# Kernel optimization log

Measured on AMD Instinct MI355X. Metric: run time of the kernel, lower is better.

Reference implementation:

```python
import jax, jax.numpy as jnp
import numpy as np

NUM_HEADS = 16


def sinusoidal_pe(N, C, dtype=jnp.float32):
    # matches the numpy construction in get_positional_encoding
    pos = jnp.arange(N, dtype=dtype)[:, None]                  # [N,1]
    dims = jnp.arange(C)                                        # [C]
    rates = 1.0 / jnp.power(jnp.asarray(10000.0, dtype), (2 * (dims // 2)).astype(dtype) / C)
    ang = pos * rates                                           # [N,C]
    pe = jnp.where(dims % 2 == 0, jnp.sin(ang), jnp.cos(ang))
    return pe.astype(dtype)


def setup_inputs() -> dict:
    key = jax.random.key(0)
    k1, k2, k3 = jax.random.split(key, 3)
    B, N, C = 4, 2048, 1024
    inputs = jax.random.normal(k1, (B, N, C), dtype=jnp.float32)
    mask_mat = jax.random.uniform(k2, (B, N), dtype=jnp.float32)
    # Glorot-uniform qkv kernel [C, 3C]
    limit = float(np.sqrt(6.0 / (C + 3 * C)))
    W_qkv = jax.random.uniform(k3, (C, 3 * C), dtype=jnp.float32, minval=-limit, maxval=limit)
    return {"inputs": inputs, "mask_mat": mask_mat, "W_qkv": W_qkv}


def reference(inputs, mask_mat, W_qkv):
    B, N, C = inputs.shape
    H = NUM_HEADS
    hd = C // H
    scale = hd ** (-0.5)

    # additive mask: -(m outer m), broadcast over heads
    neg_mask = -(mask_mat[:, :, None] * mask_mat[:, None, :])   # [B,N,N]

    x = inputs + sinusoidal_pe(N, C, inputs.dtype)              # APE
    qkv = jnp.einsum('bnc,cd->bnd', x, W_qkv)                   # [B,N,3C]
    qkv = qkv.reshape(B, N, 3, H, hd).transpose(2, 0, 3, 1, 4)  # [3,B,H,N,hd]
    q, k, v = qkv[0], qkv[1], qkv[2]

    attn = jnp.einsum('bhnd,bhmd->bhnm', q, k) * scale          # [B,H,N,N]
    attn = attn + neg_mask[:, None, :, :]
    attn = jax.nn.softmax(attn, axis=-1)
    out = jnp.einsum('bhnm,bhmd->bhnd', attn, v)                # [B,H,N,hd]
    return out.transpose(0, 2, 1, 3).reshape(B, N, C)
```

## Files before the change

kernel.cpp:

```cpp
#include <hip/hip_runtime.h>
#include <hip/hip_bf16.h>

typedef unsigned short u16;
typedef __bf16 bf16x8 __attribute__((ext_vector_type(8)));
typedef float floatx4 __attribute__((ext_vector_type(4)));

#define B_ 4
#define N_ 2048
#define C_ 1024
#define H_ 16
#define HD_ 64

__device__ __forceinline__ float b2f(u16 u) {
    union { float f; unsigned int i; } v; v.i = ((unsigned int)u) << 16; return v.f;
}
__device__ __forceinline__ u16 f2b(float f) {
    union { float f; unsigned int i; } v; v.f = f;
    unsigned int i = v.i;
    unsigned int r = i + 0x7FFFu + ((i >> 16) & 1u);
    return (u16)(r >> 16);
}
__device__ __forceinline__ unsigned int pk2(float a, float b) {
    __hip_bfloat162 t = __float22bfloat162_rn(float2{a, b});
    unsigned int u; __builtin_memcpy(&u, &t, 4); return u;
}
__device__ __forceinline__ void async16(const u16* g, u16* l) {
    __builtin_amdgcn_global_load_lds((const __attribute__((address_space(1))) unsigned int*)g,
                                     (__attribute__((address_space(3))) unsigned int*)l,
                                     16, 0, 0);
}

__global__ __launch_bounds__(256) void pe_add_kernel(const float* __restrict__ in,
                                                     u16* __restrict__ x) {
    int idx = blockIdx.x * 256 + threadIdx.x;
    int cp  = idx & 511;
    int row = idx >> 9;
    int n   = row & (N_ - 1);
    float r = exp2f(-13.287712379549449f * ((float)cp * (1.0f / 512.0f)));
    float ang = (float)n * r;
    float s, c;
    sincosf(ang, &s, &c);
    float2 pr = ((const float2*)in)[idx];
    unsigned int o = ((unsigned int)f2b(pr.y + c) << 16) | (unsigned int)f2b(pr.x + s);
    ((unsigned int*)x)[idx] = o;
}

__global__ __launch_bounds__(256) void wt_kernel(const float* __restrict__ W,
                                                 u16* __restrict__ Wt) {
    __shared__ u16 tile[32][33];
    int bx = blockIdx.x;
    int by = blockIdx.y;
    int tx = threadIdx.x & 31;
    int ty = threadIdx.x >> 5;
    for (int i = 0; i < 32; i += 8)
        tile[ty + i][tx] = f2b(W[(size_t)(by * 32 + ty + i) * 3072 + bx * 32 + tx]);
    __syncthreads();
    for (int i = 0; i < 32; i += 8)
        Wt[(size_t)(bx * 32 + ty + i) * 1024 + by * 32 + tx] = tile[tx][ty + i];
}

__global__ __launch_bounds__(256) void qkv_gemm_kernel(const u16* __restrict__ X,
                                                       const u16* __restrict__ Wt,
                                                       u16* __restrict__ q,
                                                       u16* __restrict__ k,
                                                       u16* __restrict__ vt) {
    __shared__ u16 As[128 * 64];
    __shared__ u16 Bs[128 * 64];
    int tid  = threadIdx.x;
    int wave = tid >> 6, lane = tid & 63, l15 = lane & 15, quad = lane >> 4;
    int m0 = blockIdx.x * 128;
    int n0 = blockIdx.y * 128;
    int wm = (wave & 1) * 64;
    int wn = (wave >> 1) * 64;

    floatx4 acc[4][4];
    for (int i = 0; i < 4; i++)
        for (int j = 0; j < 4; j++)
            acc[i][j] = floatx4{0.f, 0.f, 0.f, 0.f};

    int rowOff = wave * 32 + (lane >> 3);
    int colSw  = ((lane & 7) ^ (lane >> 3)) * 8;
    const u16* gA = X  + (size_t)(m0 + rowOff) * 1024 + colSw;
    const u16* gB = Wt + (size_t)(n0 + rowOff) * 1024 + colSw;
    u16* lA = As + wave * 2048;
    u16* lB = Bs + wave * 2048;

    int swl = l15 & 7;
    int aB0 = (wm + l15) * 64 + ((quad ^ swl) * 8);
    int aB1 = (wm + l15) * 64 + (((4 + quad) ^ swl) * 8);
    int bB0 = (wn + l15) * 64 + ((quad ^ swl) * 8);
    int bB1 = (wn + l15) * 64 + (((4 + quad) ^ swl) * 8);

    for (int k0 = 0; k0 < 1024; k0 += 64) {
        __syncthreads();
        async16(gA + k0,             lA);
        async16(gA + k0 +  8 * 1024, lA + 512);
        async16(gA + k0 + 16 * 1024, lA + 1024);
        async16(gA + k0 + 24 * 1024, lA + 1536);
        async16(gB + k0,             lB);
        async16(gB + k0 +  8 * 1024, lB + 512);
        async16(gB + k0 + 16 * 1024, lB + 1024);
        async16(gB + k0 + 24 * 1024, lB + 1536);
        __syncthreads();

        bf16x8 af[4][2], bf[4][2];
        for (int i = 0; i < 4; i++) {
            af[i][0] = *(const bf16x8*)(As + aB0 + i * 16 * 64);
            af[i][1] = *(const bf16x8*)(As + aB1 + i * 16 * 64);
        }
        for (int j = 0; j < 4; j++) {
            bf[j][0] = *(const bf16x8*)(Bs + bB0 + j * 16 * 64);
            bf[j][1] = *(const bf16x8*)(Bs + bB1 + j * 16 * 64);
        }
        for (int i = 0; i < 4; i++)
            for (int j = 0; j < 4; j++) {
                acc[i][j] = __builtin_amdgcn_mfma_f32_16x16x32_bf16(af[i][0], bf[j][0], acc[i][j], 0, 0, 0);
                acc[i][j] = __builtin_amdgcn_mfma_f32_16x16x32_bf16(af[i][1], bf[j][1], acc[i][j], 0, 0, 0);
            }
    }

    const float QSC = 0.125f * 1.44269504f;
    for (int i = 0; i < 4; i++) {
        int gm   = m0 + wm + i * 16 + quad * 4;
        int b    = gm >> 11;
        int nloc = gm & 2047;
        for (int j = 0; j < 4; j++) {
            int gn    = n0 + wn + j * 16 + l15;
            int which = gn >> 10;
            int cc    = gn & 1023;
            int h     = cc >> 6;
            int d     = cc & 63;
            size_t bh = (size_t)(b * 16 + h);
            if (which == 2) {
                ushort4 w4;
                w4.x = f2b(acc[i][j][0]);
                w4.y = f2b(acc[i][j][1]);
                w4.z = f2b(acc[i][j][2]);
                w4.w = f2b(acc[i][j][3]);
                *(ushort4*)(vt + (bh * 64 + d) * 2048 + nloc) = w4;
            } else {
                u16* dst = (which == 0) ? q : k;
                float sc = (which == 0) ? QSC : 1.0f;
                for (int r = 0; r < 4; r++)
                    dst[(bh * 2048 + nloc + r) * 64 + d] = f2b(acc[i][j][r] * sc);
            }
        }
    }
}

__global__ __launch_bounds__(256, 4) void attn_kernel(const u16* __restrict__ q,
                                                      const u16* __restrict__ k,
                                                      const u16* __restrict__ vt,
                                                      const float* __restrict__ mask,
                                                      float* __restrict__ out) {
    __shared__ u16 Ks[64 * 72];
    __shared__ u16 Vs[64 * 72];
    __shared__ u16 Ps[4][32 * 72];

    int tid  = threadIdx.x;
    int wave = tid >> 6, lane = tid & 63, l15 = lane & 15, quad = lane >> 4;
    int bh = blockIdx.y, b = bh >> 4, h = bh & 15;
    size_t base = (size_t)bh * (N_ * 64);
    int q0 = blockIdx.x * 128 + wave * 32;
    const float* mkb = mask + b * N_;

    bf16x8 qf[2][2];
    for (int s = 0; s < 2; s++)
        for (int dc = 0; dc < 2; dc++)
            qf[s][dc] = *(const bf16x8*)(q + base + (size_t)(q0 + s * 16 + l15) * 64 + dc * 32 + quad * 8);

    const float L2E = 1.44269504f;
    float nmq[2];
    nmq[0] = -L2E * mkb[q0 + l15];
    nmq[1] = -L2E * mkb[q0 + 16 + l15];

    floatx4 acc[2][4];
    for (int s = 0; s < 2; s++)
        for (int dt = 0; dt < 4; dt++)
            acc[s][dt] = floatx4{0.f, 0.f, 0.f, 0.f};
    float lp[2] = {0.f, 0.f};

    int r_st = tid >> 2;
    int c_st = (tid & 3) * 16;
    u16* Pw = Ps[wave];

    for (int kt = 0; kt < N_; kt += 64) {
        int4 ka = *(const int4*)(k  + base + (size_t)(kt + r_st) * 64 + c_st);
        int4 kb = *(const int4*)(k  + base + (size_t)(kt + r_st) * 64 + c_st + 8);
        int4 va = *(const int4*)(vt + ((size_t)bh * 64 + r_st) * 2048 + kt + c_st);
        int4 vb = *(const int4*)(vt + ((size_t)bh * 64 + r_st) * 2048 + kt + c_st + 8);
        float4 mkv[4];
        for (int t = 0; t < 4; t++)
            mkv[t] = *(const float4*)(mkb + kt + t * 16 + quad * 4);
        __syncthreads();
        *(int4*)(Ks + r_st * 72 + c_st)     = ka;
        *(int4*)(Ks + r_st * 72 + c_st + 8) = kb;
        *(int4*)(Vs + r_st * 72 + c_st)     = va;
        *(int4*)(Vs + r_st * 72 + c_st + 8) = vb;
        __syncthreads();

        for (int t = 0; t < 4; t++) {
            bf16x8 kf0 = *(const bf16x8*)(Ks + (t * 16 + l15) * 72 + quad * 8);
            bf16x8 kf1 = *(const bf16x8*)(Ks + (t * 16 + l15) * 72 + 32 + quad * 8);
            for (int s = 0; s < 2; s++) {
                floatx4 sa = floatx4{0.f, 0.f, 0.f, 0.f};
                sa = __builtin_amdgcn_mfma_f32_16x16x32_bf16(kf0, qf[s][0], sa, 0, 0, 0);
                sa = __builtin_amdgcn_mfma_f32_16x16x32_bf16(kf1, qf[s][1], sa, 0, 0, 0);
                float p0 = exp2f(fmaf(nmq[s], mkv[t].x, sa[0]));
                float p1 = exp2f(fmaf(nmq[s], mkv[t].y, sa[1]));
                float p2 = exp2f(fmaf(nmq[s], mkv[t].z, sa[2]));
                float p3 = exp2f(fmaf(nmq[s], mkv[t].w, sa[3]));
                lp[s] += (p0 + p1) + (p2 + p3);
                uint2 w; w.x = pk2(p0, p1); w.y = pk2(p2, p3);
                *(uint2*)(Pw + (s * 16 + l15) * 72 + t * 16 + quad * 4) = w;
            }
        }

        bf16x8 pf[2][2];
        for (int s = 0; s < 2; s++) {
            pf[s][0] = *(const bf16x8*)(Pw + (s * 16 + l15) * 72 + quad * 8);
            pf[s][1] = *(const bf16x8*)(Pw + (s * 16 + l15) * 72 + 32 + quad * 8);
        }
        for (int dt = 0; dt < 4; dt++) {
            bf16x8 vf0 = *(const bf16x8*)(Vs + (dt * 16 + l15) * 72 + quad * 8);
            bf16x8 vf1 = *(const bf16x8*)(Vs + (dt * 16 + l15) * 72 + 32 + quad * 8);
            for (int s = 0; s < 2; s++) {
                acc[s][dt] = __builtin_amdgcn_mfma_f32_16x16x32_bf16(pf[s][0], vf0, acc[s][dt], 0, 0, 0);
                acc[s][dt] = __builtin_amdgcn_mfma_f32_16x16x32_bf16(pf[s][1], vf1, acc[s][dt], 0, 0, 0);
            }
        }
    }

    for (int s = 0; s < 2; s++) {
        float lf = lp[s];
        lf += __shfl_xor(lf, 16);
        lf += __shfl_xor(lf, 32);
        float invl = 1.0f / lf;
        for (int r = 0; r < 4; r++) {
            float ir = __shfl(invl, (lane & 48) | (quad * 4 + r));
            int qrow = q0 + s * 16 + quad * 4 + r;
            float* orow = out + ((size_t)(b * N_ + qrow)) * C_ + h * 64;
            for (int dt = 0; dt < 4; dt++)
                orow[dt * 16 + l15] = acc[s][dt][r] * ir;
        }
    }
}

extern "C" void kernel_launch(void* const* d_in, const int* in_sizes, int n_in,
                              void* d_out, int out_size, void* d_ws, size_t ws_size,
                              hipStream_t stream) {
    const float* inp  = (const float*)d_in[0];
    const float* mask = (const float*)d_in[1];
    const float* W    = (const float*)d_in[2];
    float* out = (float*)d_out;

    char* ws = (char*)d_ws;
    u16* x  = (u16*)ws;
    u16* Wt = (u16*)(ws + 16777216);
    u16* q  = (u16*)(ws + 23068672);
    u16* k  = q + 8388608;
    u16* vt = k + 8388608;

    pe_add_kernel<<<16384, 256, 0, stream>>>(inp, x);
    wt_kernel<<<dim3(96, 32), 256, 0, stream>>>(W, Wt);
    qkv_gemm_kernel<<<dim3(64, 24), 256, 0, stream>>>(x, Wt, q, k, vt);
    attn_kernel<<<dim3(16, 64), 256, 0, stream>>>(q, k, vt, mask, out);
}
```

Before: 270.2 us.

## Double-buffer K/V tiles in attention and double per-wave query rows

The attention kernel now double-buffers K and V tiles in shared memory. The next tile is prefetched into registers while the current one is used, which cuts the loop to one barrier per iteration. Each wave now handles 64 query rows instead of 32, so each K/V tile is reused across twice as many rows, and the grid is halved to 512 blocks. In exchange it uses more registers and LDS, drops the occupancy hint to 2 blocks per SM, and leaves fewer blocks to fill the GPU.

```diff
diff --git a/kernel.cpp b/kernel.cpp
--- a/kernel.cpp
+++ b/kernel.cpp
@@ -148,90 +148,109 @@
     }
 }
 
-__global__ __launch_bounds__(256, 4) void attn_kernel(const u16* __restrict__ q,
+__global__ __launch_bounds__(256, 2) void attn_kernel(const u16* __restrict__ q,
                                                       const u16* __restrict__ k,
                                                       const u16* __restrict__ vt,
                                                       const float* __restrict__ mask,
                                                       float* __restrict__ out) {
-    __shared__ u16 Ks[64 * 72];
-    __shared__ u16 Vs[64 * 72];
-    __shared__ u16 Ps[4][32 * 72];
+    __shared__ u16 Ks[2][64 * 72];
+    __shared__ u16 Vs[2][64 * 72];
+    __shared__ u16 Ps[4][64 * 72];
 
     int tid  = threadIdx.x;
     int wave = tid >> 6, lane = tid & 63, l15 = lane & 15, quad = lane >> 4;
     int bh = blockIdx.y, b = bh >> 4, h = bh & 15;
     size_t base = (size_t)bh * (N_ * 64);
-    int q0 = blockIdx.x * 128 + wave * 32;
+    int q0 = blockIdx.x * 256 + wave * 64;
     const float* mkb = mask + b * N_;
 
-    bf16x8 qf[2][2];
-    for (int s = 0; s < 2; s++)
+    bf16x8 qf[4][2];
+    for (int s = 0; s < 4; s++)
         for (int dc = 0; dc < 2; dc++)
             qf[s][dc] = *(const bf16x8*)(q + base + (size_t)(q0 + s * 16 + l15) * 64 + dc * 32 + quad * 8);
 
     const float L2E = 1.44269504f;
-    float nmq[2];
-    nmq[0] = -L2E * mkb[q0 + l15];
-    nmq[1] = -L2E * mkb[q0 + 16 + l15];
-
-    floatx4 acc[2][4];
-    for (int s = 0; s < 2; s++)
+    float nmq[4];
+    for (int s = 0; s < 4; s++)
+        nmq[s] = -L2E * mkb[q0 + s * 16 + l15];
+
+    floatx4 acc[4][4];
+    for (int s = 0; s < 4; s++)
         for (int dt = 0; dt < 4; dt++)
             acc[s][dt] = floatx4{0.f, 0.f, 0.f, 0.f};
-    float lp[2] = {0.f, 0.f};
+    float lp[4] = {0.f, 0.f, 0.f, 0.f};
 
     int r_st = tid >> 2;
     int c_st = (tid & 3) * 16;
     u16* Pw = Ps[wave];
+    const u16* kgb = k  + base + (size_t)r_st * 64 + c_st;
+    const u16* vgb = vt + ((size_t)bh * 64 + r_st) * 2048 + c_st;
+
+    int4 ka, kb, va, vb;
+    ka = *(const int4*)(kgb);          kb = *(const int4*)(kgb + 8);
+    va = *(const int4*)(vgb);          vb = *(const int4*)(vgb + 8);
+    *(int4*)(Ks[0] + r_st * 72 + c_st)     = ka;
+    *(int4*)(Ks[0] + r_st * 72 + c_st + 8) = kb;
+    *(int4*)(Vs[0] + r_st * 72 + c_st)     = va;
+    *(int4*)(Vs[0] + r_st * 72 + c_st + 8) = vb;
+    ka = *(const int4*)(kgb + (size_t)64 * 64);  kb = *(const int4*)(kgb + (size_t)64 * 64 + 8);
+    va = *(const int4*)(vgb + 64);               vb = *(const int4*)(vgb + 64 + 8);
+    __syncthreads();
 
     for (int kt = 0; kt < N_; kt += 64) {
-        int4 ka = *(const int4*)(k  + base + (size_t)(kt + r_st) * 64 + c_st);
-        int4 kb = *(const int4*)(k  + base + (size_t)(kt + r_st) * 64 + c_st + 8);
-        int4 va = *(const int4*)(vt + ((size_t)bh * 64 + r_st) * 2048 + kt + c_st);
-        int4 vb = *(const int4*)(vt + ((size_t)bh * 64 + r_st) * 2048 + kt + c_st + 8);
-        float4 mkv[4];
-        for (int t = 0; t < 4; t++)
-            mkv[t] = *(const float4*)(mkb + kt + t * 16 + quad * 4);
-        __syncthreads();
-        *(int4*)(Ks + r_st * 72 + c_st)     = ka;
-        *(int4*)(Ks + r_st * 72 + c_st + 8) = kb;
-        *(int4*)(Vs + r_st * 72 + c_st)     = va;
-        *(int4*)(Vs + r_st * 72 + c_st + 8) = vb;
-        __syncthreads();
+        int bufi = (kt >> 6) & 1;
+        const u16* Kb = Ks[bufi];
+        const u16* Vb = Vs[bufi];
 
         for (int t = 0; t < 4; t++) {
-            bf16x8 kf0 = *(const bf16x8*)(Ks + (t * 16 + l15) * 72 + quad * 8);
-            bf16x8 kf1 = *(const bf16x8*)(Ks + (t * 16 + l15) * 72 + 32 + quad * 8);
-            for (int s = 0; s < 2; s++) {
+            bf16x8 kf0 = *(const bf16x8*)(Kb + (t * 16 + l15) * 72 + quad * 8);
+            bf16x8 kf1 = *(const bf16x8*)(Kb + (t * 16 + l15) * 72 + 32 + quad * 8);
+            float4 mkv = *(const float4*)(mkb + kt + t * 16 + quad * 4);
+            for (int s = 0; s < 4; s++) {
                 floatx4 sa = floatx4{0.f, 0.f, 0.f, 0.f};
                 sa = __builtin_amdgcn_mfma_f32_16x16x32_bf16(kf0, qf[s][0], sa, 0, 0, 0);
                 sa = __builtin_amdgcn_mfma_f32_16x16x32_bf16(kf1, qf[s][1], sa, 0, 0, 0);
-                float p0 = exp2f(fmaf(nmq[s], mkv[t].x, sa[0]));
-                float p1 = exp2f(fmaf(nmq[s], mkv[t].y, sa[1]));
-                float p2 = exp2f(fmaf(nmq[s], mkv[t].z, sa[2]));
-                float p3 = exp2f(fmaf(nmq[s], mkv[t].w, sa[3]));
+                float p0 = exp2f(fmaf(nmq[s], mkv.x, sa[0]));
+                float p1 = exp2f(fmaf(nmq[s], mkv.y, sa[1]));
+                float p2 = exp2f(fmaf(nmq[s], mkv.z, sa[2]));
+                float p3 = exp2f(fmaf(nmq[s], mkv.w, sa[3]));
                 lp[s] += (p0 + p1) + (p2 + p3);
                 uint2 w; w.x = pk2(p0, p1); w.y = pk2(p2, p3);
                 *(uint2*)(Pw + (s * 16 + l15) * 72 + t * 16 + quad * 4) = w;
             }
         }
 
-        bf16x8 pf[2][2];
-        for (int s = 0; s < 2; s++) {
+        bf16x8 pf[4][2];
+        for (int s = 0; s < 4; s++) {
             pf[s][0] = *(const bf16x8*)(Pw + (s * 16 + l15) * 72 + quad * 8);
             pf[s][1] = *(const bf16x8*)(Pw + (s * 16 + l15) * 72 + 32 + quad * 8);
         }
         for (int dt = 0; dt < 4; dt++) {
-            bf16x8 vf0 = *(const bf16x8*)(Vs + (dt * 16 + l15) * 72 + quad * 8);
-            bf16x8 vf1 = *(const bf16x8*)(Vs + (dt * 16 + l15) * 72 + 32 + quad * 8);
-            for (int s = 0; s < 2; s++) {
+            bf16x8 vf0 = *(const bf16x8*)(Vb + (dt * 16 + l15) * 72 + quad * 8);
+            bf16x8 vf1 = *(const bf16x8*)(Vb + (dt * 16 + l15) * 72 + 32 + quad * 8);
+            for (int s = 0; s < 4; s++) {
                 acc[s][dt] = __builtin_amdgcn_mfma_f32_16x16x32_bf16(pf[s][0], vf0, acc[s][dt], 0, 0, 0);
                 acc[s][dt] = __builtin_amdgcn_mfma_f32_16x16x32_bf16(pf[s][1], vf1, acc[s][dt], 0, 0, 0);
             }
         }
-    }
-
-    for (int s = 0; s < 2; s++) {
+
+        if (kt + 64 < N_) {
+            u16* Kn = Ks[bufi ^ 1];
+            u16* Vn = Vs[bufi ^ 1];
+            *(int4*)(Kn + r_st * 72 + c_st)     = ka;
+            *(int4*)(Kn + r_st * 72 + c_st + 8) = kb;
+            *(int4*)(Vn + r_st * 72 + c_st)     = va;
+            *(int4*)(Vn + r_st * 72 + c_st + 8) = vb;
+            if (kt + 128 < N_) {
+                size_t ko = (size_t)(kt + 128) * 64;
+                ka = *(const int4*)(kgb + ko);      kb = *(const int4*)(kgb + ko + 8);
+                va = *(const int4*)(vgb + kt + 128); vb = *(const int4*)(vgb + kt + 128 + 8);
+            }
+            __syncthreads();
+        }
+    }
+
+    for (int s = 0; s < 4; s++) {
         float lf = lp[s];
         lf += __shfl_xor(lf, 16);
         lf += __shfl_xor(lf, 32);
@@ -264,5 +283,5 @@
     pe_add_kernel<<<16384, 256, 0, stream>>>(inp, x);
     wt_kernel<<<dim3(96, 32), 256, 0, stream>>>(W, Wt);
     qkv_gemm_kernel<<<dim3(64, 24), 256, 0, stream>>>(x, Wt, q, k, vt);
-    attn_kernel<<<dim3(16, 64), 256, 0, stream>>>(q, k, vt, mask, out);
-}
+    attn_kernel<<<dim3(8, 64), 256, 0, stream>>>(q, k, vt, mask, out);
+}
```

Measured after the change: 278.7 us. 1.03x slower.
